# Performance work log

Hardware: AMD Instinct MI355X
Metric: run time of the kernel (lower is better)

Reference implementation:

```python
import jax, jax.numpy as jnp
import numpy as np

NUM_HEADS = 16


def setup_inputs() -> dict:
    key = jax.random.key(0)
    ks = jax.random.split(key, 5)
    b, s, d = 2, 2048, 1024
    std = (2.0 / (d + d)) ** 0.5
    x = jax.random.normal(ks[0], (b, s, d), dtype=jnp.float32)
    Wq = jax.random.normal(ks[1], (d, d), dtype=jnp.float32) * std
    Wk = jax.random.normal(ks[2], (d, d), dtype=jnp.float32) * std
    Wv = jax.random.normal(ks[3], (d, d), dtype=jnp.float32) * std
    Wo = jax.random.normal(ks[4], (d, d), dtype=jnp.float32) * std
    return {"x": x, "Wq": Wq, "Wk": Wk, "Wv": Wv, "Wo": Wo}


def reference(x, Wq, Wk, Wv, Wo):
    b, s, d = x.shape
    h = NUM_HEADS
    dk = d // h
    # projections: bias-free x @ W (W is [in, out])
    def split_heads(t):
        return t.reshape(b, s, h, dk).transpose(0, 2, 1, 3)  # b h s dk
    q = split_heads(x @ Wq)
    k = split_heads(x @ Wk)
    v = split_heads(x @ Wv)
    scale = 1.0 / jnp.sqrt(jnp.asarray(dk, dtype=x.dtype))
    scores = jnp.einsum('bhqd,bhkd->bhqk', q, k) * scale  # b h s s
    causal = jnp.tril(jnp.ones((s, s), dtype=bool))
    scores = jnp.where(causal, scores, -jnp.inf)
    probs = jax.nn.softmax(scores, axis=-1)
    out = jnp.einsum('bhqk,bhkd->bhqd', probs, v)
    out = out.transpose(0, 2, 1, 3).reshape(b, s, d)  # b s (h dk)
    return out @ Wo
```

## Files before the change

### kernel.cpp

```cpp
#include <hip/hip_runtime.h>

typedef unsigned short u16;
typedef unsigned int   u32;

using bf16x8 = __attribute__((ext_vector_type(8))) __bf16;
using bf16x4 = __attribute__((ext_vector_type(4))) __bf16;
using f32x4  = __attribute__((ext_vector_type(4))) float;
using s16x4  = __attribute__((ext_vector_type(4))) short;

#define NH    16
#define DKH   64
#define SEQ   2048
#define BAT   2
#define DMOD  1024

#define QSCALE 0.18033688011112042f

__device__ __forceinline__ u16 f2bf(float f) {
  union { float f; u32 u; } v; v.f = f;
  u32 r = v.u + 0x7fffu + ((v.u >> 16) & 1u);
  return (u16)(r >> 16);
}

__device__ __forceinline__ u32 pack2bf(float a, float b) {
  union { float f; u32 u; } x, y; x.f = a; y.f = b;
  u32 ua = x.u + 0x7fffu + ((x.u >> 16) & 1u);
  u32 ub = y.u + 0x7fffu + ((y.u >> 16) & 1u);
  return __builtin_amdgcn_perm(ub, ua, 0x07060302u);
}

__device__ __forceinline__ s16x4 pk4bf(float a, float b, float c, float d) {
  union { bf16x4 bv; s16x4 sv; } u;
  u.bv[0] = (__bf16)a; u.bv[1] = (__bf16)b; u.bv[2] = (__bf16)c; u.bv[3] = (__bf16)d;
  return u.sv;
}

#if __has_builtin(__builtin_amdgcn_exp2f)
#define EXP2(x) __builtin_amdgcn_exp2f(x)
#else
#define EXP2(x) exp2f(x)
#endif

#if __has_builtin(__builtin_amdgcn_mfma_f32_16x16x16bf16_1k)
__device__ __forceinline__ f32x4 mfma16(s16x4 a, s16x4 b, f32x4 c) {
  return __builtin_amdgcn_mfma_f32_16x16x16bf16_1k(a, b, c, 0, 0, 0);
}
#else
__device__ __forceinline__ f32x4 mfma16(s16x4 a, s16x4 b, f32x4 c) {
  f32x4 d;
  asm volatile("v_mfma_f32_16x16x16_bf16 %0, %1, %2, %3\n\ts_nop 7\n\ts_nop 7"
               : "=v"(d) : "v"(a), "v"(b), "v"(c));
  return d;
}
#endif

typedef const __attribute__((address_space(1))) u32 glb_u32;
typedef __attribute__((address_space(3))) u32 lds_u32;
__device__ __forceinline__ void gload16(const u16* g, u16* l) {
  __builtin_amdgcn_global_load_lds((glb_u32*)(const void*)g, (lds_u32*)(void*)l, 16, 0, 0);
}

__global__ __launch_bounds__(256) void transpose_all(const float* __restrict__ Wq,
                                                     const float* __restrict__ Wk,
                                                     const float* __restrict__ Wv,
                                                     const float* __restrict__ Wo,
                                                     u16* __restrict__ Wt) {
  __shared__ u16 t[32][33];
  const float* W = blockIdx.z == 0 ? Wq : blockIdx.z == 1 ? Wk : blockIdx.z == 2 ? Wv : Wo;
  u16* o = Wt + (size_t)blockIdx.z * DMOD * DMOD;
  int bx = blockIdx.x * 32, by = blockIdx.y * 32;
  int x = threadIdx.x, y = threadIdx.y;
  #pragma unroll
  for (int i = 0; i < 32; i += 8)
    t[y + i][x] = f2bf(W[(size_t)(by + y + i) * DMOD + bx + x]);
  __syncthreads();
  #pragma unroll
  for (int i = 0; i < 32; i += 8)
    o[(size_t)(bx + y + i) * DMOD + by + x] = t[x][y + i];
}

__global__ __launch_bounds__(256) void convert_x(const float* __restrict__ x,
                                                 u16* __restrict__ xb) {
  size_t i = ((size_t)blockIdx.x * 256 + threadIdx.x) * 8;
  float4 f0 = *(const float4*)(x + i);
  float4 f1 = *(const float4*)(x + i + 4);
  uint4 o;
  o.x = pack2bf(f0.x, f0.y); o.y = pack2bf(f0.z, f0.w);
  o.z = pack2bf(f1.x, f1.y); o.w = pack2bf(f1.z, f1.w);
  *(uint4*)(xb + i) = o;
}

__global__ __launch_bounds__(256, 3) void gemm_qkv(const u16* __restrict__ A,
                                                   const u16* __restrict__ Bt,
                                                   u16* __restrict__ Qo,
                                                   u16* __restrict__ Ko,
                                                   u16* __restrict__ Vo) {
  __shared__ __align__(16) u16 As[128 * 64];
  __shared__ __align__(16) u16 Bs[128 * 64];
  const int tid  = threadIdx.x;
  const int lane = tid & 63, wv = tid >> 6;
  const int wm   = wv >> 1, wn = wv & 1;
  const int lrow = lane & 15, quad = lane >> 4;
  const int tileM = blockIdx.x * 128, tileN = blockIdx.y * 128;

  const f32x4 fz = {0.f, 0.f, 0.f, 0.f};
  f32x4 acc[4][4];
  #pragma unroll
  for (int i = 0; i < 4; ++i)
    #pragma unroll
    for (int j = 0; j < 4; ++j) acc[i][j] = fz;

  for (int kt = 0; kt < DMOD; kt += 64) {
    if (kt) __syncthreads();
    #pragma unroll
    for (int i = 0; i < 4; ++i) {
      int idx = i * 256 + tid;
      int r = idx >> 3, c = idx & 7;
      gload16(&A [(size_t)(tileM + r) * DMOD + kt + ((c ^ (r & 7)) << 3)], &As[idx * 8]);
      gload16(&Bt[(size_t)(tileN + r) * DMOD + kt + ((c ^ (r & 7)) << 3)], &Bs[idx * 8]);
    }
    __syncthreads();

    #pragma unroll
    for (int kk = 0; kk < 2; ++kk) {
      bf16x8 af[4], bfr[4];
      #pragma unroll
      for (int mt = 0; mt < 4; ++mt)
        af[mt] = *(const bf16x8*)(&As[(wm * 64 + mt * 16 + lrow) * 64
                                      + (((kk * 4 + quad) ^ (lrow & 7)) << 3)]);
      #pragma unroll
      for (int nt = 0; nt < 4; ++nt)
        bfr[nt] = *(const bf16x8*)(&Bs[(wn * 64 + nt * 16 + lrow) * 64
                                       + (((kk * 4 + quad) ^ (lrow & 7)) << 3)]);
      #pragma unroll
      for (int mt = 0; mt < 4; ++mt)
        #pragma unroll
        for (int nt = 0; nt < 4; ++nt)
          acc[mt][nt] = __builtin_amdgcn_mfma_f32_16x16x32_bf16(af[mt], bfr[nt],
                                                                acc[mt][nt], 0, 0, 0);
    }
  }

  #pragma unroll
  for (int mt = 0; mt < 4; ++mt) {
    #pragma unroll
    for (int nt = 0; nt < 4; ++nt) {
      int gm0 = tileM + wm * 64 + mt * 16 + quad * 4;
      int gn  = tileN + wn * 64 + nt * 16 + lrow;
      int which = gn >> 10, col = gn & 1023;
      int bb = gm0 >> 11, srw0 = gm0 & (SEQ - 1);
      int hh = col >> 6, dki = col & (DKH - 1);
      size_t bhi = (size_t)(bb * NH + hh);
      if (which == 0) {
        #pragma unroll
        for (int r = 0; r < 4; ++r)
          Qo[(bhi * SEQ + srw0 + r) * DKH + dki] = f2bf(acc[mt][nt][r] * QSCALE);
      } else if (which == 1) {
        #pragma unroll
        for (int r = 0; r < 4; ++r)
          Ko[(bhi * SEQ + srw0 + r) * DKH + dki] = f2bf(acc[mt][nt][r]);
      } else {
        uint2 pk;
        pk.x = pack2bf(acc[mt][nt][0], acc[mt][nt][1]);
        pk.y = pack2bf(acc[mt][nt][2], acc[mt][nt][3]);
        *(uint2*)(&Vo[(((bhi * (SEQ / 4)) + (srw0 >> 2)) * DKH + dki) * 4]) = pk;
      }
    }
  }
}

__global__ __launch_bounds__(256, 3) void gemm_out(const u16* __restrict__ A,
                                                   const u16* __restrict__ Bt,
                                                   float* __restrict__ Co) {
  __shared__ __align__(16) u16 As[128 * 64];
  __shared__ __align__(16) u16 Bs[64 * 64];
  const int tid  = threadIdx.x;
  const int lane = tid & 63, wv = tid >> 6;
  const int wm   = wv & 1, wn = wv >> 1;
  const int lrow = lane & 15, quad = lane >> 4;
  const int tileM = blockIdx.x * 128, tileN = blockIdx.y * 64;

  const f32x4 fz = {0.f, 0.f, 0.f, 0.f};
  f32x4 acc[4][2];
  #pragma unroll
  for (int i = 0; i < 4; ++i) { acc[i][0] = fz; acc[i][1] = fz; }

  for (int kt = 0; kt < DMOD; kt += 64) {
    if (kt) __syncthreads();
    #pragma unroll
    for (int i = 0; i < 4; ++i) {
      int idx = i * 256 + tid;
      int r = idx >> 3, c = idx & 7;
      gload16(&A[(size_t)(tileM + r) * DMOD + kt + ((c ^ (r & 7)) << 3)], &As[idx * 8]);
    }
    #pragma unroll
    for (int i = 0; i < 2; ++i) {
      int idx = i * 256 + tid;
      int r = idx >> 3, c = idx & 7;
      gload16(&Bt[(size_t)(tileN + r) * DMOD + kt + ((c ^ (r & 7)) << 3)], &Bs[idx * 8]);
    }
    __syncthreads();

    #pragma unroll
    for (int kk = 0; kk < 2; ++kk) {
      bf16x8 af[4], bfr[2];
      #pragma unroll
      for (int mt = 0; mt < 4; ++mt)
        af[mt] = *(const bf16x8*)(&As[(wm * 64 + mt * 16 + lrow) * 64
                                      + (((kk * 4 + quad) ^ (lrow & 7)) << 3)]);
      #pragma unroll
      for (int nt = 0; nt < 2; ++nt)
        bfr[nt] = *(const bf16x8*)(&Bs[(wn * 32 + nt * 16 + lrow) * 64
                                       + (((kk * 4 + quad) ^ (lrow & 7)) << 3)]);
      #pragma unroll
      for (int mt = 0; mt < 4; ++mt)
        #pragma unroll
        for (int nt = 0; nt < 2; ++nt)
          acc[mt][nt] = __builtin_amdgcn_mfma_f32_16x16x32_bf16(af[mt], bfr[nt],
                                                                acc[mt][nt], 0, 0, 0);
    }
  }

  #pragma unroll
  for (int mt = 0; mt < 4; ++mt)
    #pragma unroll
    for (int nt = 0; nt < 2; ++nt)
      #pragma unroll
      for (int r = 0; r < 4; ++r) {
        int gm = tileM + wm * 64 + mt * 16 + quad * 4 + r;
        int gn = tileN + wn * 32 + nt * 16 + lrow;
        Co[(size_t)gm * DMOD + gn] = acc[mt][nt][r];
      }
}

#define OPAD 68

__global__ __launch_bounds__(256, 2) void attn_k(const u16* __restrict__ Q,
                                                 const u16* __restrict__ Kg,
                                                 const u16* __restrict__ Vg,
                                                 u16* __restrict__ Og) {
  __shared__ __align__(16) u16 Ksb[2][2][64 * 64];
  __shared__ __align__(16) u16 Vsb[2][2][16 * 256];
  __shared__ __align__(16) u16 Osc[64 * OPAD];
  __shared__ float Lsc[32];

  const int tid  = threadIdx.x;
  const int lane = tid & 63, w = tid >> 6;
  const int g    = w >> 1,  wg = w & 1;
  const int lrow = lane & 15, quad = lane >> 4;
  const int bh = blockIdx.x, y = blockIdx.y;
  const int b = bh >> 4, h = bh & 15;
  const int qB = 31 - y;
  const int sAend = y >> 1;

  const u16* Qbh = Q  + (size_t)bh * SEQ * DKH;
  const u16* Kbh = Kg + (size_t)bh * SEQ * DKH;
  const u16* Vbh = Vg + (size_t)bh * SEQ * DKH;

  const f32x4 fz = {0.f, 0.f, 0.f, 0.f};
  f32x4 oacc[2][4];
  float lsum[2];
  bf16x8 bq[2][2];

#define DEC(s_, g_, qt_, j_, v_)                                                   \
  { if ((s_) <= sAend) { qt_ = y;  j_ = 2 * (s_) + (g_);              v_ = (j_ <= y);  } \
    else               { qt_ = qB; j_ = 2 * ((s_) - sAend - 1) + (g_); v_ = (j_ <= qB); } }

#define STAGE1(gg, p_, j_)                                                          \
  { _Pragma("unroll")                                                               \
    for (int i_ = 0; i_ < 2; ++i_) {                                                \
      int cD = i_ * 256 + tid; int r_ = cD >> 3, c_ = cD & 7;                       \
      gload16(&Kbh[(size_t)((j_) * 64 + r_) * DKH + ((c_ ^ (r_ & 7)) << 3)],        \
              &Ksb[gg][p_][cD * 8]); }                                              \
    _Pragma("unroll")                                                               \
    for (int i_ = 0; i_ < 2; ++i_) {                                                \
      int cD = i_ * 256 + tid; int sq_ = cD >> 5, c_ = cD & 31;                     \
      gload16(&Vbh[(size_t)((j_) * 16 + sq_) * 256 + ((c_ ^ (sq_ & 7)) << 3)],      \
              &Vsb[gg][p_][cD * 8]); } }

#define LOADQ(qt_)                                                                  \
  { _Pragma("unroll")                                                               \
    for (int s_ = 0; s_ < 2; ++s_)                                                  \
      _Pragma("unroll")                                                             \
      for (int kk_ = 0; kk_ < 2; ++kk_)                                             \
        bq[s_][kk_] = *(const bf16x8*)(&Qbh[(size_t)((qt_) * 64 + wg * 32 + s_ * 16 \
                                            + lrow) * DKH + kk_ * 32 + quad * 8]); }

  auto EPI = [&](int qt) {
    float ls[2];
    #pragma unroll
    for (int s2 = 0; s2 < 2; ++s2) {
      float v = lsum[s2];
      v += __shfl_xor(v, 16, 64);
      v += __shfl_xor(v, 32, 64);
      ls[s2] = v;
    }
    float* OscF = (float*)Osc;
    #pragma unroll
    for (int ph = 0; ph < 2; ++ph) {
      if (g == 1) {
        int srow = wg * 16 + lrow;
        #pragma unroll
        for (int d = 0; d < 4; ++d)
          *(f32x4*)(&OscF[srow * OPAD + d * 16 + quad * 4]) = oacc[ph][d];
        if (quad == 0) Lsc[srow] = ls[ph];
      }
      __syncthreads();
      if (g == 0) {
        int srow = wg * 16 + lrow;
        ls[ph] += Lsc[srow];
        #pragma unroll
        for (int d = 0; d < 4; ++d) {
          f32x4 ov = *(const f32x4*)(&OscF[srow * OPAD + d * 16 + quad * 4]);
          oacc[ph][d] += ov;
        }
      }
      __syncthreads();
    }
    if (g == 0) {
      #pragma unroll
      for (int s2 = 0; s2 < 2; ++s2) {
        float inv = 1.f / ls[s2];
        int row = wg * 32 + s2 * 16 + lrow;
        #pragma unroll
        for (int d = 0; d < 4; ++d) {
          uint2 pkk;
          pkk.x = pack2bf(oacc[s2][d][0] * inv, oacc[s2][d][1] * inv);
          pkk.y = pack2bf(oacc[s2][d][2] * inv, oacc[s2][d][3] * inv);
          *(uint2*)(&Osc[row * OPAD + d * 16 + quad * 4]) = pkk;
        }
      }
    }
    __syncthreads();
    #pragma unroll
    for (int k2 = 0; k2 < 2; ++k2) {
      int c2 = k2 * 256 + tid;
      int row = c2 >> 3, ch = c2 & 7;
      uint4 vv = *(const uint4*)(&Osc[row * OPAD + ch * 8]);
      *(uint4*)(&Og[(size_t)(b * SEQ + qt * 64 + row) * DMOD + h * DKH + ch * 8]) = vv;
    }
  };

  { int qt0, j0; bool v0;
    DEC(0, 0, qt0, j0, v0); if (v0) STAGE1(0, 0, j0);
    DEC(0, 1, qt0, j0, v0); if (v0) STAGE1(1, 0, j0);
  }
  LOADQ(y);
  #pragma unroll
  for (int s2 = 0; s2 < 2; ++s2) {
    oacc[s2][0] = fz; oacc[s2][1] = fz; oacc[s2][2] = fz; oacc[s2][3] = fz;
    lsum[s2] = 0.f;
  }
  __syncthreads();

  for (int s = 0; s <= 16; ++s) {
    const int p = s & 1;

    if (s < 16) {
      int qtn, jn; bool vn;
      DEC(s + 1, 0, qtn, jn, vn); if (vn) STAGE1(0, p ^ 1, jn);
      DEC(s + 1, 1, qtn, jn, vn); if (vn) STAGE1(1, p ^ 1, jn);
    }

    int qt, j; bool valid;
    DEC(s, g, qt, j, valid);
    if (valid) {
      const u16* Ks = Ksb[g][p];
      const u16* Vs = Vsb[g][p];
      if (j < qt) {
        __builtin_amdgcn_s_setprio(1);
        f32x4 sacc[2][4];
        #pragma unroll
        for (int s2 = 0; s2 < 2; ++s2)
          #pragma unroll
          for (int m = 0; m < 4; ++m) sacc[s2][m] = fz;
        #pragma unroll
        for (int kk = 0; kk < 2; ++kk)
          #pragma unroll
          for (int m = 0; m < 4; ++m) {
            bf16x8 ak = *(const bf16x8*)(&Ks[(m * 16 + lrow) * 64
                                             + (((kk * 4 + quad) ^ (lrow & 7)) << 3)]);
            sacc[0][m] = __builtin_amdgcn_mfma_f32_16x16x32_bf16(ak, bq[0][kk], sacc[0][m], 0, 0, 0);
            sacc[1][m] = __builtin_amdgcn_mfma_f32_16x16x32_bf16(ak, bq[1][kk], sacc[1][m], 0, 0, 0);
          }
        #pragma unroll
        for (int m = 0; m < 4; ++m) {
          float p00 = EXP2(sacc[0][m][0]), p01 = EXP2(sacc[0][m][1]);
          float p02 = EXP2(sacc[0][m][2]), p03 = EXP2(sacc[0][m][3]);
          float p10 = EXP2(sacc[1][m][0]), p11 = EXP2(sacc[1][m][1]);
          float p12 = EXP2(sacc[1][m][2]), p13 = EXP2(sacc[1][m][3]);
          lsum[0] += (p00 + p01) + (p02 + p03);
          lsum[1] += (p10 + p11) + (p12 + p13);
          s16x4 pk0 = pk4bf(p00, p01, p02, p03);
          s16x4 pk1 = pk4bf(p10, p11, p12, p13);
          const int sq = m * 4 + quad;
          #pragma unroll
          for (int d = 0; d < 4; ++d) {
            int dk = d * 16 + lrow;
            s16x4 av = *(const s16x4*)(&Vs[sq * 256
                                           + ((((dk >> 1) ^ (sq & 7)) << 3) | ((dk & 1) << 2))]);
            oacc[0][d] = mfma16(av, pk0, oacc[0][d]);
            oacc[1][d] = mfma16(av, pk1, oacc[1][d]);
          }
        }
        __builtin_amdgcn_s_setprio(0);
      } else {
        #pragma unroll
        for (int s2 = 0; s2 < 2; ++s2) {
          const int L = 2 * wg + s2;
          for (int m = 0; m < L; ++m) {
            f32x4 sv = fz;
            #pragma unroll
            for (int kk = 0; kk < 2; ++kk) {
              bf16x8 ak = *(const bf16x8*)(&Ks[(m * 16 + lrow) * 64
                                               + (((kk * 4 + quad) ^ (lrow & 7)) << 3)]);
              sv = __builtin_amdgcn_mfma_f32_16x16x32_bf16(ak, bq[s2][kk], sv, 0, 0, 0);
            }
            float p0 = EXP2(sv[0]), p1 = EXP2(sv[1]), p2 = EXP2(sv[2]), p3 = EXP2(sv[3]);
            lsum[s2] += (p0 + p1) + (p2 + p3);
            s16x4 pk = pk4bf(p0, p1, p2, p3);
            const int sq = m * 4 + quad;
            #pragma unroll
            for (int d = 0; d < 4; ++d) {
              int dk = d * 16 + lrow;
              s16x4 av = *(const s16x4*)(&Vs[sq * 256
                                             + ((((dk >> 1) ^ (sq & 7)) << 3) | ((dk & 1) << 2))]);
              oacc[s2][d] = mfma16(av, pk, oacc[s2][d]);
            }
          }
          {
            f32x4 sv = fz;
            #pragma unroll
            for (int kk = 0; kk < 2; ++kk) {
              bf16x8 ak = *(const bf16x8*)(&Ks[(L * 16 + lrow) * 64
                                               + (((kk * 4 + quad) ^ (lrow & 7)) << 3)]);
              sv = __builtin_amdgcn_mfma_f32_16x16x32_bf16(ak, bq[s2][kk], sv, 0, 0, 0);
            }
            float pp[4];
            #pragma unroll
            for (int r = 0; r < 4; ++r)
              pp[r] = (quad * 4 + r > lrow) ? 0.f : EXP2(sv[r]);
            lsum[s2] += (pp[0] + pp[1]) + (pp[2] + pp[3]);
            s16x4 pk = pk4bf(pp[0], pp[1], pp[2], pp[3]);
            const int sq = L * 4 + quad;
            #pragma unroll
            for (int d = 0; d < 4; ++d) {
              int dk = d * 16 + lrow;
              s16x4 av = *(const s16x4*)(&Vs[sq * 256
                                             + ((((dk >> 1) ^ (sq & 7)) << 3) | ((dk & 1) << 2))]);
              oacc[s2][d] = mfma16(av, pk, oacc[s2][d]);
            }
          }
        }
      }
    }

    __syncthreads();

    if (s == sAend) {
      EPI(y);
      #pragma unroll
      for (int s2 = 0; s2 < 2; ++s2) {
        oacc[s2][0] = fz; oacc[s2][1] = fz; oacc[s2][2] = fz; oacc[s2][3] = fz;
        lsum[s2] = 0.f;
      }
      LOADQ(qB);
    } else if (s == 16) {
      EPI(qB);
    }
  }
#undef DEC
#undef STAGE1
#undef LOADQ
}

extern "C" void kernel_launch(void* const* d_in, const int* in_sizes, int n_in,
                              void* d_out, int out_size, void* d_ws, size_t ws_size,
                              hipStream_t stream) {
  const float* x  = (const float*)d_in[0];
  const float* Wq = (const float*)d_in[1];
  const float* Wk = (const float*)d_in[2];
  const float* Wv = (const float*)d_in[3];
  const float* Wo = (const float*)d_in[4];

  u16* ws = (u16*)d_ws;
  const size_t WSZ = (size_t)DMOD * DMOD;
  const size_t TSZ = (size_t)BAT * NH * SEQ * DKH;
  u16* Wt  = ws;
  u16* Wto = Wt + 3 * WSZ;
  u16* xb  = Wt + 4 * WSZ;
  u16* Qb  = xb + TSZ;
  u16* Kb  = Qb + TSZ;
  u16* Vb  = Kb + TSZ;
  u16* Ob  = xb;

  transpose_all<<<dim3(32, 32, 4), dim3(32, 8), 0, stream>>>(Wq, Wk, Wv, Wo, Wt);
  convert_x<<<dim3(2048), 256, 0, stream>>>(x, xb);

  gemm_qkv<<<dim3(32, 24), 256, 0, stream>>>(xb, Wt, Qb, Kb, Vb);

  attn_k<<<dim3(32, 16), 256, 0, stream>>>(Qb, Kb, Vb, Ob);

  gemm_out<<<dim3(32, 16), 256, 0, stream>>>(Ob, Wto, (float*)d_out);
}
```

Before: 164.4 us.

## Merge weight transpose and x conversion into one launch; remap QKV GEMM tiles per XCD

Combines the weight transpose/convert kernel and the x-to-bf16 conversion into a single prep launch, using a fifth z-slice of blocks that each convert 16 elements per thread. It also remaps gemm_qkv block IDs so that blocks landing on the same XCD (round-robin by block id mod 8) cover a contiguous 8x12 sub-grid of M/N tiles. The remap is meant to improve L2 reuse of A and B tiles within each XCD's cache. Together these remove one launch and aim to reduce redundant HBM traffic in the projection GEMM.

```diff
diff --git a/kernel.cpp b/kernel.cpp
--- a/kernel.cpp
+++ b/kernel.cpp
@@ -60,34 +60,41 @@
   __builtin_amdgcn_global_load_lds((glb_u32*)(const void*)g, (lds_u32*)(void*)l, 16, 0, 0);
 }
 
-__global__ __launch_bounds__(256) void transpose_all(const float* __restrict__ Wq,
-                                                     const float* __restrict__ Wk,
-                                                     const float* __restrict__ Wv,
-                                                     const float* __restrict__ Wo,
-                                                     u16* __restrict__ Wt) {
-  __shared__ u16 t[32][33];
-  const float* W = blockIdx.z == 0 ? Wq : blockIdx.z == 1 ? Wk : blockIdx.z == 2 ? Wv : Wo;
-  u16* o = Wt + (size_t)blockIdx.z * DMOD * DMOD;
-  int bx = blockIdx.x * 32, by = blockIdx.y * 32;
-  int x = threadIdx.x, y = threadIdx.y;
-  #pragma unroll
-  for (int i = 0; i < 32; i += 8)
-    t[y + i][x] = f2bf(W[(size_t)(by + y + i) * DMOD + bx + x]);
-  __syncthreads();
-  #pragma unroll
-  for (int i = 0; i < 32; i += 8)
-    o[(size_t)(bx + y + i) * DMOD + by + x] = t[x][y + i];
-}
-
-__global__ __launch_bounds__(256) void convert_x(const float* __restrict__ x,
-                                                 u16* __restrict__ xb) {
-  size_t i = ((size_t)blockIdx.x * 256 + threadIdx.x) * 8;
-  float4 f0 = *(const float4*)(x + i);
-  float4 f1 = *(const float4*)(x + i + 4);
-  uint4 o;
-  o.x = pack2bf(f0.x, f0.y); o.y = pack2bf(f0.z, f0.w);
-  o.z = pack2bf(f1.x, f1.y); o.w = pack2bf(f1.z, f1.w);
-  *(uint4*)(xb + i) = o;
+__global__ __launch_bounds__(256) void prep(const float* __restrict__ Wq,
+                                            const float* __restrict__ Wk,
+                                            const float* __restrict__ Wv,
+                                            const float* __restrict__ Wo,
+                                            u16* __restrict__ Wt,
+                                            const float* __restrict__ x,
+                                            u16* __restrict__ xb) {
+  const int z = blockIdx.z;
+  if (z < 4) {
+    __shared__ u16 t[32][33];
+    const float* W = z == 0 ? Wq : z == 1 ? Wk : z == 2 ? Wv : Wo;
+    u16* o = Wt + (size_t)z * DMOD * DMOD;
+    int bx = blockIdx.x * 32, by = blockIdx.y * 32;
+    int tx = threadIdx.x, ty = threadIdx.y;
+    #pragma unroll
+    for (int i = 0; i < 32; i += 8)
+      t[ty + i][tx] = f2bf(W[(size_t)(by + ty + i) * DMOD + bx + tx]);
+    __syncthreads();
+    #pragma unroll
+    for (int i = 0; i < 32; i += 8)
+      o[(size_t)(bx + ty + i) * DMOD + by + tx] = t[tx][ty + i];
+  } else {
+    int cid = blockIdx.x + 32 * blockIdx.y;
+    int tid1 = threadIdx.y * 32 + threadIdx.x;
+    size_t i = ((size_t)cid * 256 + tid1) * 16;
+    #pragma unroll
+    for (int half = 0; half < 2; ++half) {
+      float4 f0 = *(const float4*)(x + i + half * 8);
+      float4 f1 = *(const float4*)(x + i + half * 8 + 4);
+      uint4 o;
+      o.x = pack2bf(f0.x, f0.y); o.y = pack2bf(f0.z, f0.w);
+      o.z = pack2bf(f1.x, f1.y); o.w = pack2bf(f1.z, f1.w);
+      *(uint4*)(xb + i + half * 8) = o;
+    }
+  }
 }
 
 __global__ __launch_bounds__(256, 3) void gemm_qkv(const u16* __restrict__ A,
@@ -101,7 +108,13 @@
   const int lane = tid & 63, wv = tid >> 6;
   const int wm   = wv >> 1, wn = wv & 1;
   const int lrow = lane & 15, quad = lane >> 4;
-  const int tileM = blockIdx.x * 128, tileN = blockIdx.y * 128;
+
+  const int bid = blockIdx.x + 32 * blockIdx.y;
+  const int xcd = bid & 7, loc = bid >> 3;
+  const int lm = loc & 7, ln = loc >> 3;
+  const int cM = xcd & 3, cN = xcd >> 2;
+  const int tileM = (cM * 8 + lm) * 128;
+  const int tileN = (cN * 12 + ln) * 128;
 
   const f32x4 fz = {0.f, 0.f, 0.f, 0.f};
   f32x4 acc[4][4];
@@ -494,8 +507,7 @@
   u16* Vb  = Kb + TSZ;
   u16* Ob  = xb;
 
-  transpose_all<<<dim3(32, 32, 4), dim3(32, 8), 0, stream>>>(Wq, Wk, Wv, Wo, Wt);
-  convert_x<<<dim3(2048), 256, 0, stream>>>(x, xb);
+  prep<<<dim3(32, 32, 5), dim3(32, 8), 0, stream>>>(Wq, Wk, Wv, Wo, Wt, x, xb);
 
   gemm_qkv<<<dim3(32, 24), 256, 0, stream>>>(xb, Wt, Qb, Kb, Vb);
 
```

Result: no change. 166.6 us (+1.3%).
